# Kernel tuning notes

Hardware: AMD Instinct MI355X
Metric: run time of the kernel (lower is better)

Reference implementation:

```python
import jax, jax.numpy as jnp
import numpy as np

ATT_DIM = 1024
N_HEADS = 16
D_HEAD = ATT_DIM // N_HEADS
LARGE = 1e30  # fp32 masking constant used by masked_softmax


def setup_inputs() -> dict:
    key = jax.random.key(0)
    ks = jax.random.split(key, 12)
    B, Tq, Tv, D = 4, 2048, 2048, 1024
    s = 1.0 / np.sqrt(D)
    sf = 1.0 / np.sqrt(ATT_DIM)
    return {
        "query": jax.random.normal(ks[0], (B, Tq, D), jnp.float32),
        "value": jax.random.normal(ks[1], (B, Tv, D), jnp.float32),
        "value_lens": jax.random.randint(ks[2], (B,), 0, Tv, jnp.int32),
        "Wq": jax.random.normal(ks[3], (D, ATT_DIM), jnp.float32) * s,
        "bq": jnp.zeros((ATT_DIM,), jnp.float32),
        "Wk": jax.random.normal(ks[4], (D, ATT_DIM), jnp.float32) * s,
        "bk": jnp.zeros((ATT_DIM,), jnp.float32),
        "Wv": jax.random.normal(ks[5], (D, ATT_DIM), jnp.float32) * s,
        "bv": jnp.zeros((ATT_DIM,), jnp.float32),
        "Wf": jax.random.normal(ks[6], (ATT_DIM, ATT_DIM), jnp.float32) * sf,
        "bf": jnp.zeros((ATT_DIM,), jnp.float32),
    }


def _attention(query, value, value_lens, Wq, bq, Wk, bk, Wv, bv, Wf, bf):
    B, Tq, _ = query.shape
    Tv = value.shape[1]
    # projections
    k = value @ Wk + bk                     # [B,Tv,att_dim]
    v = value @ Wv + bv                     # [B,Tv,att_dim]
    q = (query @ Wq + bq) / jnp.sqrt(jnp.asarray(D_HEAD, query.dtype))
    # split heads
    q = q.reshape(B, Tq, N_HEADS, D_HEAD)
    k = k.reshape(B, Tv, N_HEADS, D_HEAD)
    v = v.reshape(B, Tv, N_HEADS, D_HEAD)
    # energy: [B, n_heads, Tq, Tv]
    energy = jnp.einsum("bind,bjnd->bnij", q, k)
    # sequence mask: [B,1,1,Tv]
    mask = (jnp.arange(Tv)[None, :] < value_lens[:, None]).astype(energy.dtype)
    energy = energy - (1.0 - mask)[:, None, None, :] * jnp.asarray(LARGE, energy.dtype)
    att_weight = jax.nn.softmax(energy, axis=-1)
    # context: [B, Tq, n_heads, d_head] -> [B, Tq, att_dim]
    context = jnp.einsum("bnij,bjnd->bind", att_weight, v).reshape(B, Tq, ATT_DIM)
    return context @ Wf + bf  # final_att (num_att_head > 1)


def reference(query, value, value_lens, Wq, bq, Wk, bk, Wv, bv, Wf, bf):
    return _attention(query, value, value_lens, Wq, bq, Wk, bk, Wv, bv, Wf, bf)
```

## Files before the change

### kernel.cpp

```cpp
#include <hip/hip_runtime.h>
#include <hip/hip_bf16.h>

typedef __attribute__((ext_vector_type(8))) short short8;
typedef __attribute__((ext_vector_type(4))) short short4b;
typedef __attribute__((ext_vector_type(4))) float f32x4;
typedef unsigned short u16;
typedef unsigned int u32;
typedef __attribute__((ext_vector_type(2))) unsigned int u32x2;
typedef __attribute__((ext_vector_type(8))) unsigned short u16x8;
typedef __attribute__((ext_vector_type(4))) unsigned short u16x4;

__device__ __forceinline__ u16 f2bf(float f) {
    u32 u = __builtin_bit_cast(u32, f);
    u += 0x7FFFu + ((u >> 16) & 1u);
    return (u16)(u >> 16);
}
__device__ __forceinline__ u32 cvtpk(float a, float b) {
    u32 r;
    asm("v_cvt_pk_bf16_f32 %0, %1, %2" : "=v"(r) : "v"(a), "v"(b));
    return r;
}
__device__ __forceinline__ float fexp2(float x) {
    float r;
    asm("v_exp_f32 %0, %1" : "=v"(r) : "v"(x));
    return r;
}
#if defined(__has_builtin)
#if __has_builtin(__builtin_amdgcn_mfma_f32_16x16x16_bf16)
#define MFMA16(a, b, c) __builtin_amdgcn_mfma_f32_16x16x16_bf16((a), (b), (c), 0, 0, 0)
#elif __has_builtin(__builtin_amdgcn_mfma_f32_16x16x16bf16_1k)
#define MFMA16(a, b, c) __builtin_amdgcn_mfma_f32_16x16x16bf16_1k((a), (b), (c), 0, 0, 0)
#endif
#endif
#ifndef MFMA16
__device__ __forceinline__ f32x4 mfma16_asm(short4b a, short4b b, f32x4 c) {
    asm volatile("s_nop 1\n\tv_mfma_f32_16x16x16_bf16 %0, %1, %2, %0"
                 : "+v"(c) : "v"(a), "v"(b));
    return c;
}
#define MFMA16(a, b, c) mfma16_asm((a), (b), (c))
#endif

__device__ __forceinline__ int swz(int row, int col) {
    return (row * 128 + col * 2) ^ ((row & 7) << 4);
}

__device__ __forceinline__ void gl16(const void* g, void* l) {
    __builtin_amdgcn_global_load_lds(
        (const __attribute__((address_space(1))) unsigned int*)g,
        (__attribute__((address_space(3))) unsigned int*)l, 16, 0, 0);
}

#define FENCE() asm volatile("" ::: "memory")
#define BARRIER() do { FENCE(); __builtin_amdgcn_s_barrier(); FENCE(); } while (0)

__global__ __launch_bounds__(256)
void prep_kernel(const float* __restrict__ query, const float* __restrict__ value,
                 u16* __restrict__ qB, u16* __restrict__ vB,
                 const float* __restrict__ W0, const float* __restrict__ W1,
                 const float* __restrict__ W2, const float* __restrict__ W3,
                 u16* __restrict__ T0, u16* __restrict__ T1,
                 u16* __restrict__ T2, u16* __restrict__ T3)
{
    int bid = blockIdx.x;
    if (bid < 8192) {
        const float* src; u16* dst;
        if (bid < 4096) { src = query; dst = qB; }
        else            { src = value; dst = vB; bid -= 4096; }
        const int i = bid * 256 + threadIdx.x;
        const float4 a = ((const float4*)src)[2 * i];
        const float4 b = ((const float4*)src)[2 * i + 1];
        u16x8 h;
        h[0] = f2bf(a.x); h[1] = f2bf(a.y); h[2] = f2bf(a.z); h[3] = f2bf(a.w);
        h[4] = f2bf(b.x); h[5] = f2bf(b.y); h[6] = f2bf(b.z); h[7] = f2bf(b.w);
        ((u16x8*)dst)[i] = h;
        return;
    }
    int b2 = bid - 8192;
    const int z = b2 >> 10; b2 &= 1023;
    const float* W; u16* T;
    switch (z) {
        case 0:  W = W0; T = T0; break;
        case 1:  W = W1; T = T1; break;
        case 2:  W = W2; T = T2; break;
        default: W = W3; T = T3; break;
    }
    __shared__ u16 tile[32][33];
    const int tid = threadIdx.x;
    const int n0 = (b2 & 31) * 32, k0 = (b2 >> 5) * 32;
    const int r = tid >> 3, c = (tid & 7) * 4;
    float4 v = *(const float4*)(W + (size_t)(k0 + r) * 1024 + n0 + c);
    tile[c + 0][r] = f2bf(v.x);
    tile[c + 1][r] = f2bf(v.y);
    tile[c + 2][r] = f2bf(v.z);
    tile[c + 3][r] = f2bf(v.w);
    __syncthreads();
    u16x4 h;
    h[0] = tile[r][c]; h[1] = tile[r][c + 1]; h[2] = tile[r][c + 2]; h[3] = tile[r][c + 3];
    *(u16x4*)(T + (size_t)(n0 + r) * 1024 + k0 + c) = h;
}

#define GNK 32

__device__ __forceinline__ void stage_a(const u16* __restrict__ A, unsigned char* bufA,
                                        int row0, int kt, int tid) {
    const int r = tid >> 2, s = tid & 3;
    gl16((const unsigned char*)A + (size_t)(row0 + r) * 2048 + kt * 64 + ((s ^ (r & 3)) << 4),
         bufA + tid * 16);
}
__device__ __forceinline__ void stage_b(const u16* __restrict__ BT, unsigned char* bufB,
                                        int col0, int kt, int hb, int tid) {
    const int r = hb * 128 + (tid >> 2), s = tid & 3;
    gl16((const unsigned char*)BT + (size_t)(col0 + r) * 2048 + kt * 64 + ((s ^ (r & 3)) << 4),
         bufB + hb * 8192 + tid * 16);
}

__device__ __forceinline__ void gemm_core(const u16* __restrict__ A, const u16* __restrict__ BT,
                                          int row0, int col0, unsigned char* smem,
                                          int tid, int wm, int wn, int l15, int lhi,
                                          f32x4 acc[4][4])
{
    const int slot = (lhi ^ (l15 & 3)) << 4;
    #pragma unroll
    for (int kt = 0; kt < 2; ++kt) {
        unsigned char* buf = smem + kt * 24576;
        stage_a(A, buf, row0, kt, tid);
        stage_b(BT, buf + 8192, col0, kt, 0, tid);
        stage_b(BT, buf + 8192, col0, kt, 1, tid);
    }
    asm volatile("s_waitcnt vmcnt(3)" ::: "memory");
    BARRIER();

    int cb = 0;
    for (int k = 0; k < GNK; ++k) {
        unsigned char* bufA = smem + cb * 24576;
        unsigned char* bufB = bufA + 8192;
        const bool st = (k + 2 < GNK);
        int nb = cb + 2; if (nb >= 3) nb -= 3;
        unsigned char* nbuf = smem + nb * 24576;
        cb = (cb == 2) ? 0 : cb + 1;

        short8 a0, a1, a2, a3, b0, b1;
        a0 = *(const short8*)(bufA + (wm * 64 + 0 * 16 + l15) * 64 + slot);
        a1 = *(const short8*)(bufA + (wm * 64 + 1 * 16 + l15) * 64 + slot);
        a2 = *(const short8*)(bufA + (wm * 64 + 2 * 16 + l15) * 64 + slot);
        a3 = *(const short8*)(bufA + (wm * 64 + 3 * 16 + l15) * 64 + slot);
        b0 = *(const short8*)(bufB + (wn * 64 + 0 * 16 + l15) * 64 + slot);
        b1 = *(const short8*)(bufB + (wn * 64 + 1 * 16 + l15) * 64 + slot);
        if (st) stage_a(A, nbuf, row0, k + 2, tid);
        BARRIER();
        __builtin_amdgcn_s_setprio(1);
        acc[0][0] = __builtin_amdgcn_mfma_f32_16x16x32_bf16(a0, b0, acc[0][0], 0, 0, 0);
        acc[0][1] = __builtin_amdgcn_mfma_f32_16x16x32_bf16(a0, b1, acc[0][1], 0, 0, 0);
        acc[1][0] = __builtin_amdgcn_mfma_f32_16x16x32_bf16(a1, b0, acc[1][0], 0, 0, 0);
        acc[1][1] = __builtin_amdgcn_mfma_f32_16x16x32_bf16(a1, b1, acc[1][1], 0, 0, 0);
        acc[2][0] = __builtin_amdgcn_mfma_f32_16x16x32_bf16(a2, b0, acc[2][0], 0, 0, 0);
        acc[2][1] = __builtin_amdgcn_mfma_f32_16x16x32_bf16(a2, b1, acc[2][1], 0, 0, 0);
        acc[3][0] = __builtin_amdgcn_mfma_f32_16x16x32_bf16(a3, b0, acc[3][0], 0, 0, 0);
        acc[3][1] = __builtin_amdgcn_mfma_f32_16x16x32_bf16(a3, b1, acc[3][1], 0, 0, 0);
        __builtin_amdgcn_s_setprio(0);
        BARRIER();

        short8 b2, b3;
        b2 = *(const short8*)(bufB + (wn * 64 + 2 * 16 + l15) * 64 + slot);
        b3 = *(const short8*)(bufB + (wn * 64 + 3 * 16 + l15) * 64 + slot);
        if (st) {
            stage_b(BT, nbuf + 8192, col0, k + 2, 0, tid);
            stage_b(BT, nbuf + 8192, col0, k + 2, 1, tid);
        }
        if (k < GNK - 2)       asm volatile("s_waitcnt vmcnt(3)" ::: "memory");
        else if (k == GNK - 2) asm volatile("s_waitcnt vmcnt(0)" ::: "memory");
        BARRIER();
        __builtin_amdgcn_s_setprio(1);
        acc[0][2] = __builtin_amdgcn_mfma_f32_16x16x32_bf16(a0, b2, acc[0][2], 0, 0, 0);
        acc[0][3] = __builtin_amdgcn_mfma_f32_16x16x32_bf16(a0, b3, acc[0][3], 0, 0, 0);
        acc[1][2] = __builtin_amdgcn_mfma_f32_16x16x32_bf16(a1, b2, acc[1][2], 0, 0, 0);
        acc[1][3] = __builtin_amdgcn_mfma_f32_16x16x32_bf16(a1, b3, acc[1][3], 0, 0, 0);
        acc[2][2] = __builtin_amdgcn_mfma_f32_16x16x32_bf16(a2, b2, acc[2][2], 0, 0, 0);
        acc[2][3] = __builtin_amdgcn_mfma_f32_16x16x32_bf16(a2, b3, acc[2][3], 0, 0, 0);
        acc[3][2] = __builtin_amdgcn_mfma_f32_16x16x32_bf16(a3, b2, acc[3][2], 0, 0, 0);
        acc[3][3] = __builtin_amdgcn_mfma_f32_16x16x32_bf16(a3, b3, acc[3][3], 0, 0, 0);
        __builtin_amdgcn_s_setprio(0);
        BARRIER();
    }
}

__global__ __launch_bounds__(512, 4)
void proj_kernel(const u16* __restrict__ queryB, const u16* __restrict__ valueB,
                 const u16* __restrict__ WqT, const u16* __restrict__ WkT,
                 const u16* __restrict__ WvT,
                 const float* __restrict__ bq, const float* __restrict__ bk,
                 const float* __restrict__ bv,
                 u16* __restrict__ Qb, u16* __restrict__ Kb, u16* __restrict__ Vt)
{
    __shared__ __align__(16) unsigned char smem[73728];
    const int t = (blockIdx.x & 7) * 96 + (blockIdx.x >> 3);
    const int z = t >> 8;
    const int tile = t & 255;
    const int row0 = (tile >> 2) * 128, col0 = (tile & 3) * 256;

    const u16* A    = (z == 0) ? queryB : valueB;
    const u16* BT   = (z == 0) ? WqT : (z == 1) ? WkT : WvT;
    const float* bias = (z == 0) ? bq : (z == 1) ? bk : bv;

    const int tid = threadIdx.x;
    const int lane = tid & 63, w = tid >> 6;
    const int wm = w >> 2, wn = w & 3;
    const int l15 = lane & 15, lhi = lane >> 4;

    f32x4 acc[4][4];
    const f32x4 fz = {0.f, 0.f, 0.f, 0.f};
    #pragma unroll
    for (int m = 0; m < 4; ++m)
        #pragma unroll
        for (int n = 0; n < 4; ++n) acc[m][n] = fz;

    gemm_core(A, BT, row0, col0, smem, tid, wm, wn, l15, lhi, acc);

    if (z < 2) {
        u16* out = (z == 0) ? Qb : Kb;
        const float scale = (z == 0) ? 0.18033688011112042f : 1.0f;
        const int bb = row0 >> 11;
        #pragma unroll
        for (int n = 0; n < 4; ++n) {
            int col = col0 + wn * 64 + n * 16 + l15;
            int hh = col >> 6, d = col & 63;
            float bv2 = bias[col];
            #pragma unroll
            for (int m = 0; m < 4; ++m) {
                int rbase = row0 + wm * 64 + m * 16 + lhi * 4;
                #pragma unroll
                for (int rr = 0; rr < 4; ++rr) {
                    int trow = (rbase + rr) & 2047;
                    out[(((size_t)bb * 16 + hh) * 2048 + trow) * 64 + d] =
                        f2bf((acc[m][n][rr] + bv2) * scale);
                }
            }
        }
    } else {
        __syncthreads();
        u16* vl = (u16*)smem;
        #pragma unroll
        for (int n = 0; n < 4; ++n) {
            int c = wn * 64 + n * 16 + l15;
            float bv2 = bias[col0 + c];
            #pragma unroll
            for (int m = 0; m < 4; ++m) {
                int rl = wm * 64 + m * 16 + lhi * 4;
                u16x4 h;
                #pragma unroll
                for (int rr = 0; rr < 4; ++rr) h[rr] = f2bf(acc[m][n][rr] + bv2);
                *(u16x4*)(vl + c * 132 + rl) = h;
            }
        }
        __syncthreads();
        const int bb = row0 >> 11, t0 = row0 & 2047;
        const int c = tid >> 1, hseg = tid & 1;
        const int col = col0 + c;
        const int hh = col >> 6, d = col & 63;
        size_t gb = (((size_t)bb * 16 + hh) * 64 + d) * 2048 + t0 + hseg * 64;
        #pragma unroll
        for (int j = 0; j < 8; ++j) {
            u16x8 v = *(const u16x8*)(vl + c * 132 + hseg * 64 + j * 8);
            *(u16x8*)(Vt + gb + j * 8) = v;
        }
    }
}

__global__ __launch_bounds__(512, 4)
void fgemm_kernel(const u16* __restrict__ Ctx, const u16* __restrict__ WfT,
                  const float* __restrict__ bias, float* __restrict__ out)
{
    __shared__ __align__(16) unsigned char smem[73728];
    const int t = (blockIdx.x & 7) * 32 + (blockIdx.x >> 3);
    const int row0 = (t >> 2) * 128, col0 = (t & 3) * 256;

    const int tid = threadIdx.x;
    const int lane = tid & 63, w = tid >> 6;
    const int wm = w >> 2, wn = w & 3;
    const int l15 = lane & 15, lhi = lane >> 4;

    f32x4 acc[4][4];
    const f32x4 fz = {0.f, 0.f, 0.f, 0.f};
    #pragma unroll
    for (int m = 0; m < 4; ++m)
        #pragma unroll
        for (int n = 0; n < 4; ++n) acc[m][n] = fz;

    gemm_core(Ctx, WfT, row0, col0, smem, tid, wm, wn, l15, lhi, acc);

    #pragma unroll
    for (int n = 0; n < 4; ++n) {
        int col = col0 + wn * 64 + n * 16 + l15;
        float bv2 = bias[col];
        #pragma unroll
        for (int m = 0; m < 4; ++m) {
            int rbase = row0 + wm * 64 + m * 16 + lhi * 4;
            #pragma unroll
            for (int rr = 0; rr < 4; ++rr)
                out[(size_t)(rbase + rr) * 1024 + col] = acc[m][n][rr] + bv2;
        }
    }
}

__global__ __launch_bounds__(512, 4)
void attn_kernel(const u16* __restrict__ Qb, const u16* __restrict__ Kb,
                 const u16* __restrict__ Vt, const int* __restrict__ lens,
                 u16* __restrict__ Ctx)
{
    __shared__ __align__(16) unsigned char ksm[2][8192];
    __shared__ __align__(16) unsigned char vsm[2][8192];

    const int tid = threadIdx.x;
    const int lane = tid & 63;
    const int w = tid >> 6;
    const int l15 = lane & 15, lhi = lane >> 4;
    const int u = blockIdx.x;
    const int b = (u >> 8) & 3;
    const int v = u & 255;
    const int qt = (v >> 3) & 15;
    const int hh = ((v >> 7) & 1) * 8 + (v & 7);
    const size_t head = (size_t)(b * 16 + hh);
    const unsigned char* Kbase = (const unsigned char*)Kb + head * (2048 * 128);
    const unsigned char* Vbase = (const unsigned char*)Vt + head * (2048 * 128);
    const unsigned char* Qbase = (const unsigned char*)Qb + head * (2048 * 128) + (size_t)qt * (128 * 128);

    const int o0 = w * 1024 + lane * 16;
    const int r0 = o0 >> 7;
    const int sc0 = (o0 & 127) ^ ((r0 & 7) << 4);

    const unsigned char* kp = Kbase + (size_t)r0 * 128 + sc0;
    const unsigned char* vp = Vbase + (size_t)r0 * 4096 + sc0;

    const int lens_b = lens[b];
    const bool uniform = (lens_b == 0);
    const int len = uniform ? 2048 : lens_b;
    const int nt = (len + 63) >> 6;
    const bool tail = (!uniform) && ((len & 63) != 0);

    auto stage = [&](int t, int bi) {
        gl16(kp + (size_t)t * 8192, ksm[bi] + o0);
        gl16(vp + (size_t)t * 128, vsm[bi] + o0);
    };
    stage(0, 0);

    short8 qa[2];
    #pragma unroll
    for (int ks = 0; ks < 2; ++ks)
        qa[ks] = *(const short8*)(Qbase + (w * 16 + l15) * 128 + ks * 64 + lhi * 16);

    short4b ones16;
    #pragma unroll
    for (int i = 0; i < 4; ++i) ones16[i] = (short)0x3F80;

    __syncthreads();

    float m = -1e30f;
    const f32x4 fz = {0.f, 0.f, 0.f, 0.f};
    f32x4 cs = fz;
    f32x4 cT[4];
    #pragma unroll
    for (int nf = 0; nf < 4; ++nf) cT[nf] = fz;

    for (int t = 0; t < nt; ++t) {
        const int cur = t & 1;
        if (t + 1 < nt) stage(t + 1, cur ^ 1);

        f32x4 s[4];
        #pragma unroll
        for (int jf = 0; jf < 4; ++jf) s[jf] = fz;
        if (!uniform) {
            __builtin_amdgcn_s_setprio(1);
            #pragma unroll
            for (int ks = 0; ks < 2; ++ks)
                #pragma unroll
                for (int jf = 0; jf < 4; ++jf) {
                    short8 kb = *(const short8*)(ksm[cur] + swz(jf * 16 + l15, ks * 32 + lhi * 8));
                    s[jf] = __builtin_amdgcn_mfma_f32_16x16x32_bf16(kb, qa[ks], s[jf], 0, 0, 0);
                }
            __builtin_amdgcn_s_setprio(0);
            if (tail && t == nt - 1) {
                const int kvb = t * 64 + lhi * 4;
                #pragma unroll
                for (int jf = 0; jf < 4; ++jf)
                    #pragma unroll
                    for (int r = 0; r < 4; ++r)
                        if (kvb + jf * 16 + r >= len) s[jf][r] = -1e30f;
            }
        }
        f32x4 m4;
        #pragma unroll
        for (int r = 0; r < 4; ++r)
            m4[r] = fmaxf(fmaxf(s[0][r], s[1][r]), fmaxf(s[2][r], s[3][r]));
        float tmax = fmaxf(fmaxf(m4[0], m4[1]), fmaxf(m4[2], m4[3]));
        tmax = fmaxf(tmax, __shfl_xor(tmax, 16));
        tmax = fmaxf(tmax, __shfl_xor(tmax, 32));
        if (__any(tmax > m + 8.f)) {
            const float mnew = fmaxf(m, tmax);
            const float sc = fexp2(m - mnew);
            #pragma unroll
            for (int r = 0; r < 4; ++r) cs[r] *= sc;
            #pragma unroll
            for (int nf = 0; nf < 4; ++nf)
                #pragma unroll
                for (int r = 0; r < 4; ++r) cT[nf][r] *= sc;
            m = mnew;
        }
        #pragma unroll
        for (int jf = 0; jf < 4; ++jf)
            #pragma unroll
            for (int r = 0; r < 4; ++r)
                s[jf][r] = fexp2(s[jf][r] - m);
        short4b pf[4];
        #pragma unroll
        for (int jf = 0; jf < 4; ++jf) {
            u32x2 t2 = { cvtpk(s[jf][0], s[jf][1]), cvtpk(s[jf][2], s[jf][3]) };
            pf[jf] = __builtin_bit_cast(short4b, t2);
        }
        __builtin_amdgcn_s_setprio(1);
        #pragma unroll
        for (int jf = 0; jf < 4; ++jf) {
            cs = MFMA16(ones16, pf[jf], cs);
            #pragma unroll
            for (int nf = 0; nf < 4; ++nf) {
                short4b vb = *(const short4b*)(vsm[cur] + swz(nf * 16 + l15, jf * 16 + lhi * 4));
                cT[nf] = MFMA16(vb, pf[jf], cT[nf]);
            }
        }
        __builtin_amdgcn_s_setprio(0);
        __syncthreads();
    }

    asm volatile("s_nop 7");
    const float inv = 1.0f / cs[0];
    const int trow = qt * 128 + w * 16 + l15;
    u16* op = Ctx + ((size_t)b * 2048 + trow) * 1024 + hh * 64 + lhi * 4;
    #pragma unroll
    for (int nf = 0; nf < 4; ++nf) {
        u16x4 h;
        #pragma unroll
        for (int r = 0; r < 4; ++r) h[r] = f2bf(cT[nf][r] * inv);
        *(u16x4*)(op + nf * 16) = h;
    }
}

extern "C" void kernel_launch(void* const* d_in, const int* in_sizes, int n_in,
                              void* d_out, int out_size, void* d_ws, size_t ws_size,
                              hipStream_t stream)
{
    (void)in_sizes; (void)n_in; (void)out_size; (void)ws_size;
    const float* query = (const float*)d_in[0];
    const float* value = (const float*)d_in[1];
    const int*   lens  = (const int*)d_in[2];
    const float* Wq = (const float*)d_in[3];
    const float* bq = (const float*)d_in[4];
    const float* Wk = (const float*)d_in[5];
    const float* bk = (const float*)d_in[6];
    const float* Wv = (const float*)d_in[7];
    const float* bv = (const float*)d_in[8];
    const float* Wf = (const float*)d_in[9];
    const float* bfp = (const float*)d_in[10];

    unsigned char* ws = (unsigned char*)d_ws;
    const size_t MB = (size_t)1 << 20;
    u16* WqT = (u16*)(ws + 0 * MB);
    u16* WkT = (u16*)(ws + 2 * MB);
    u16* WvT = (u16*)(ws + 4 * MB);
    u16* WfT = (u16*)(ws + 6 * MB);
    u16* Qb  = (u16*)(ws + 8 * MB);
    u16* Kb  = (u16*)(ws + 24 * MB);
    u16* Vt  = (u16*)(ws + 40 * MB);
    u16* Ctx = (u16*)(ws + 56 * MB);

    u16* queryB = (u16*)d_out;
    u16* valueB = queryB + (size_t)8192 * 1024;

    prep_kernel<<<dim3(12288), dim3(256), 0, stream>>>(query, value, queryB, valueB,
                                                       Wq, Wk, Wv, Wf, WqT, WkT, WvT, WfT);

    proj_kernel<<<dim3(768), dim3(512), 0, stream>>>(queryB, valueB, WqT, WkT, WvT,
                                                     bq, bk, bv, Qb, Kb, Vt);

    attn_kernel<<<dim3(1024), dim3(512), 0, stream>>>(Qb, Kb, Vt, lens, Ctx);

    fgemm_kernel<<<dim3(256), dim3(512), 0, stream>>>(Ctx, WfT, bfp, (float*)d_out);
}
```

Baseline: 173.9 us.

## Shrink GEMM tiles to 128x128 and simplify the pipeline to one barrier phase

The projection and final GEMMs now use 128x128 output tiles instead of 128x256, which doubles the grid size (1536 and 512 blocks) and cuts shared memory per block from 72KB to 48KB. The K-loop is restructured so that all loads for a stage are issued up front, followed by a single wait and barrier per iteration, instead of two split phases. The aim is better occupancy and load balance across CUs, especially for the 256-block final GEMM. The cost is lower data reuse per tile, which means more global and L2 traffic for the B operand.

After: 180.8 us. +4.0%, slower.

```diff
diff --git a/kernel.cpp b/kernel.cpp
--- a/kernel.cpp
+++ b/kernel.cpp
@@ -102,53 +102,53 @@
 
 #define GNK 32
 
-__device__ __forceinline__ void stage_a(const u16* __restrict__ A, unsigned char* bufA,
-                                        int row0, int kt, int tid) {
+__device__ __forceinline__ void stg_a(const u16* __restrict__ A, unsigned char* buf,
+                                      int row0, int kt, int tid) {
     const int r = tid >> 2, s = tid & 3;
     gl16((const unsigned char*)A + (size_t)(row0 + r) * 2048 + kt * 64 + ((s ^ (r & 3)) << 4),
-         bufA + tid * 16);
-}
-__device__ __forceinline__ void stage_b(const u16* __restrict__ BT, unsigned char* bufB,
-                                        int col0, int kt, int hb, int tid) {
-    const int r = hb * 128 + (tid >> 2), s = tid & 3;
+         buf + tid * 16);
+}
+__device__ __forceinline__ void stg_b(const u16* __restrict__ BT, unsigned char* buf,
+                                      int col0, int kt, int tid) {
+    const int r = tid >> 2, s = tid & 3;
     gl16((const unsigned char*)BT + (size_t)(col0 + r) * 2048 + kt * 64 + ((s ^ (r & 3)) << 4),
-         bufB + hb * 8192 + tid * 16);
-}
-
-__device__ __forceinline__ void gemm_core(const u16* __restrict__ A, const u16* __restrict__ BT,
-                                          int row0, int col0, unsigned char* smem,
-                                          int tid, int wm, int wn, int l15, int lhi,
-                                          f32x4 acc[4][4])
+         buf + 8192 + tid * 16);
+}
+
+__device__ __forceinline__ void gemm128(const u16* __restrict__ A, const u16* __restrict__ BT,
+                                        int row0, int col0, unsigned char* smem,
+                                        int tid, int wm, int wn, int l15, int lhi,
+                                        f32x4 acc[4][2])
 {
     const int slot = (lhi ^ (l15 & 3)) << 4;
-    #pragma unroll
-    for (int kt = 0; kt < 2; ++kt) {
-        unsigned char* buf = smem + kt * 24576;
-        stage_a(A, buf, row0, kt, tid);
-        stage_b(BT, buf + 8192, col0, kt, 0, tid);
-        stage_b(BT, buf + 8192, col0, kt, 1, tid);
-    }
-    asm volatile("s_waitcnt vmcnt(3)" ::: "memory");
+    stg_a(A, smem, row0, 0, tid);
+    stg_b(BT, smem, col0, 0, tid);
+    stg_a(A, smem + 16384, row0, 1, tid);
+    stg_b(BT, smem + 16384, col0, 1, tid);
+    asm volatile("s_waitcnt vmcnt(2)" ::: "memory");
     BARRIER();
 
     int cb = 0;
     for (int k = 0; k < GNK; ++k) {
-        unsigned char* bufA = smem + cb * 24576;
+        unsigned char* bufA = smem + cb * 16384;
         unsigned char* bufB = bufA + 8192;
-        const bool st = (k + 2 < GNK);
         int nb = cb + 2; if (nb >= 3) nb -= 3;
-        unsigned char* nbuf = smem + nb * 24576;
         cb = (cb == 2) ? 0 : cb + 1;
-
+        if (k + 2 < GNK) {
+            unsigned char* nbuf = smem + nb * 16384;
+            stg_a(A, nbuf, row0, k + 2, tid);
+            stg_b(BT, nbuf, col0, k + 2, tid);
+        }
+        if (k < GNK - 2)       asm volatile("s_waitcnt vmcnt(2)" ::: "memory");
+        else if (k == GNK - 2) asm volatile("s_waitcnt vmcnt(0)" ::: "memory");
+        BARRIER();
         short8 a0, a1, a2, a3, b0, b1;
         a0 = *(const short8*)(bufA + (wm * 64 + 0 * 16 + l15) * 64 + slot);
         a1 = *(const short8*)(bufA + (wm * 64 + 1 * 16 + l15) * 64 + slot);
         a2 = *(const short8*)(bufA + (wm * 64 + 2 * 16 + l15) * 64 + slot);
         a3 = *(const short8*)(bufA + (wm * 64 + 3 * 16 + l15) * 64 + slot);
-        b0 = *(const short8*)(bufB + (wn * 64 + 0 * 16 + l15) * 64 + slot);
-        b1 = *(const short8*)(bufB + (wn * 64 + 1 * 16 + l15) * 64 + slot);
-        if (st) stage_a(A, nbuf, row0, k + 2, tid);
-        BARRIER();
+        b0 = *(const short8*)(bufB + (wn * 32 + 0 * 16 + l15) * 64 + slot);
+        b1 = *(const short8*)(bufB + (wn * 32 + 1 * 16 + l15) * 64 + slot);
         __builtin_amdgcn_s_setprio(1);
         acc[0][0] = __builtin_amdgcn_mfma_f32_16x16x32_bf16(a0, b0, acc[0][0], 0, 0, 0);
         acc[0][1] = __builtin_amdgcn_mfma_f32_16x16x32_bf16(a0, b1, acc[0][1], 0, 0, 0);
@@ -160,28 +160,6 @@
         acc[3][1] = __builtin_amdgcn_mfma_f32_16x16x32_bf16(a3, b1, acc[3][1], 0, 0, 0);
         __builtin_amdgcn_s_setprio(0);
         BARRIER();
-
-        short8 b2, b3;
-        b2 = *(const short8*)(bufB + (wn * 64 + 2 * 16 + l15) * 64 + slot);
-        b3 = *(const short8*)(bufB + (wn * 64 + 3 * 16 + l15) * 64 + slot);
-        if (st) {
-            stage_b(BT, nbuf + 8192, col0, k + 2, 0, tid);
-            stage_b(BT, nbuf + 8192, col0, k + 2, 1, tid);
-        }
-        if (k < GNK - 2)       asm volatile("s_waitcnt vmcnt(3)" ::: "memory");
-        else if (k == GNK - 2) asm volatile("s_waitcnt vmcnt(0)" ::: "memory");
-        BARRIER();
-        __builtin_amdgcn_s_setprio(1);
-        acc[0][2] = __builtin_amdgcn_mfma_f32_16x16x32_bf16(a0, b2, acc[0][2], 0, 0, 0);
-        acc[0][3] = __builtin_amdgcn_mfma_f32_16x16x32_bf16(a0, b3, acc[0][3], 0, 0, 0);
-        acc[1][2] = __builtin_amdgcn_mfma_f32_16x16x32_bf16(a1, b2, acc[1][2], 0, 0, 0);
-        acc[1][3] = __builtin_amdgcn_mfma_f32_16x16x32_bf16(a1, b3, acc[1][3], 0, 0, 0);
-        acc[2][2] = __builtin_amdgcn_mfma_f32_16x16x32_bf16(a2, b2, acc[2][2], 0, 0, 0);
-        acc[2][3] = __builtin_amdgcn_mfma_f32_16x16x32_bf16(a2, b3, acc[2][3], 0, 0, 0);
-        acc[3][2] = __builtin_amdgcn_mfma_f32_16x16x32_bf16(a3, b2, acc[3][2], 0, 0, 0);
-        acc[3][3] = __builtin_amdgcn_mfma_f32_16x16x32_bf16(a3, b3, acc[3][3], 0, 0, 0);
-        __builtin_amdgcn_s_setprio(0);
-        BARRIER();
     }
 }
 
@@ -193,11 +171,11 @@
                  const float* __restrict__ bv,
                  u16* __restrict__ Qb, u16* __restrict__ Kb, u16* __restrict__ Vt)
 {
-    __shared__ __align__(16) unsigned char smem[73728];
-    const int t = (blockIdx.x & 7) * 96 + (blockIdx.x >> 3);
-    const int z = t >> 8;
-    const int tile = t & 255;
-    const int row0 = (tile >> 2) * 128, col0 = (tile & 3) * 256;
+    __shared__ __align__(16) unsigned char smem[49152];
+    const int t = (blockIdx.x & 7) * 192 + (blockIdx.x >> 3);
+    const int z = t >> 9;
+    const int tile = t & 511;
+    const int row0 = (tile >> 3) * 128, col0 = (tile & 7) * 128;
 
     const u16* A    = (z == 0) ? queryB : valueB;
     const u16* BT   = (z == 0) ? WqT : (z == 1) ? WkT : WvT;
@@ -208,22 +186,22 @@
     const int wm = w >> 2, wn = w & 3;
     const int l15 = lane & 15, lhi = lane >> 4;
 
-    f32x4 acc[4][4];
+    f32x4 acc[4][2];
     const f32x4 fz = {0.f, 0.f, 0.f, 0.f};
     #pragma unroll
     for (int m = 0; m < 4; ++m)
         #pragma unroll
-        for (int n = 0; n < 4; ++n) acc[m][n] = fz;
-
-    gemm_core(A, BT, row0, col0, smem, tid, wm, wn, l15, lhi, acc);
+        for (int n = 0; n < 2; ++n) acc[m][n] = fz;
+
+    gemm128(A, BT, row0, col0, smem, tid, wm, wn, l15, lhi, acc);
 
     if (z < 2) {
         u16* out = (z == 0) ? Qb : Kb;
         const float scale = (z == 0) ? 0.18033688011112042f : 1.0f;
         const int bb = row0 >> 11;
         #pragma unroll
-        for (int n = 0; n < 4; ++n) {
-            int col = col0 + wn * 64 + n * 16 + l15;
+        for (int n = 0; n < 2; ++n) {
+            int col = col0 + wn * 32 + n * 16 + l15;
             int hh = col >> 6, d = col & 63;
             float bv2 = bias[col];
             #pragma unroll
@@ -241,26 +219,26 @@
         __syncthreads();
         u16* vl = (u16*)smem;
         #pragma unroll
-        for (int n = 0; n < 4; ++n) {
-            int c = wn * 64 + n * 16 + l15;
+        for (int n = 0; n < 2; ++n) {
+            int c = wn * 32 + n * 16 + l15;
             float bv2 = bias[col0 + c];
             #pragma unroll
             for (int m = 0; m < 4; ++m) {
                 int rl = wm * 64 + m * 16 + lhi * 4;
-                u16x4 h;
+                u16x4 hv;
                 #pragma unroll
-                for (int rr = 0; rr < 4; ++rr) h[rr] = f2bf(acc[m][n][rr] + bv2);
-                *(u16x4*)(vl + c * 132 + rl) = h;
+                for (int rr = 0; rr < 4; ++rr) hv[rr] = f2bf(acc[m][n][rr] + bv2);
+                *(u16x4*)(vl + c * 132 + rl) = hv;
             }
         }
         __syncthreads();
         const int bb = row0 >> 11, t0 = row0 & 2047;
-        const int c = tid >> 1, hseg = tid & 1;
+        const int c = tid >> 2, hseg = tid & 1, jh = (tid >> 1) & 1;
         const int col = col0 + c;
         const int hh = col >> 6, d = col & 63;
         size_t gb = (((size_t)bb * 16 + hh) * 64 + d) * 2048 + t0 + hseg * 64;
         #pragma unroll
-        for (int j = 0; j < 8; ++j) {
+        for (int j = jh * 4; j < jh * 4 + 4; ++j) {
             u16x8 v = *(const u16x8*)(vl + c * 132 + hseg * 64 + j * 8);
             *(u16x8*)(Vt + gb + j * 8) = v;
         }
@@ -271,27 +249,27 @@
 void fgemm_kernel(const u16* __restrict__ Ctx, const u16* __restrict__ WfT,
                   const float* __restrict__ bias, float* __restrict__ out)
 {
-    __shared__ __align__(16) unsigned char smem[73728];
-    const int t = (blockIdx.x & 7) * 32 + (blockIdx.x >> 3);
-    const int row0 = (t >> 2) * 128, col0 = (t & 3) * 256;
+    __shared__ __align__(16) unsigned char smem[49152];
+    const int t = (blockIdx.x & 7) * 64 + (blockIdx.x >> 3);
+    const int row0 = (t >> 3) * 128, col0 = (t & 7) * 128;
 
     const int tid = threadIdx.x;
     const int lane = tid & 63, w = tid >> 6;
     const int wm = w >> 2, wn = w & 3;
     const int l15 = lane & 15, lhi = lane >> 4;
 
-    f32x4 acc[4][4];
+    f32x4 acc[4][2];
     const f32x4 fz = {0.f, 0.f, 0.f, 0.f};
     #pragma unroll
     for (int m = 0; m < 4; ++m)
         #pragma unroll
-        for (int n = 0; n < 4; ++n) acc[m][n] = fz;
-
-    gemm_core(Ctx, WfT, row0, col0, smem, tid, wm, wn, l15, lhi, acc);
-
-    #pragma unroll
-    for (int n = 0; n < 4; ++n) {
-        int col = col0 + wn * 64 + n * 16 + l15;
+        for (int n = 0; n < 2; ++n) acc[m][n] = fz;
+
+    gemm128(Ctx, WfT, row0, col0, smem, tid, wm, wn, l15, lhi, acc);
+
+    #pragma unroll
+    for (int n = 0; n < 2; ++n) {
+        int col = col0 + wn * 32 + n * 16 + l15;
         float bv2 = bias[col];
         #pragma unroll
         for (int m = 0; m < 4; ++m) {
@@ -478,10 +456,10 @@
     prep_kernel<<<dim3(12288), dim3(256), 0, stream>>>(query, value, queryB, valueB,
                                                        Wq, Wk, Wv, Wf, WqT, WkT, WvT, WfT);
 
-    proj_kernel<<<dim3(768), dim3(512), 0, stream>>>(queryB, valueB, WqT, WkT, WvT,
-                                                     bq, bk, bv, Qb, Kb, Vt);
+    proj_kernel<<<dim3(1536), dim3(512), 0, stream>>>(queryB, valueB, WqT, WkT, WvT,
+                                                      bq, bk, bv, Qb, Kb, Vt);
 
     attn_kernel<<<dim3(1024), dim3(512), 0, stream>>>(Qb, Kb, Vt, lens, Ctx);
 
-    fgemm_kernel<<<dim3(256), dim3(512), 0, stream>>>(Ctx, WfT, bfp, (float*)d_out);
-}
+    fgemm_kernel<<<dim3(512), dim3(512), 0, stream>>>(Ctx, WfT, bfp, (float*)d_out);
+}
```

## Schedule attention tiles through an atomic work queue, longest batches first

Applied to the files above, without the earlier changes.

The attention kernel no longer maps each block to a fixed (batch, head, q-tile). Blocks now pull tile indices from a global atomic counter, and tiles are ordered so that batches with the most KV tiles (from value_lens) are handed out first. The aim is to reduce load imbalance and tail idle time, since KV lengths differ per batch. The cost is an atomic plus an extra barrier per tile, a changed head/q-tile traversal order that may affect L2 reuse, and a completion counter that resets state on the assumption that exactly 1024 blocks run.

Result: slower. 194.2 us (+11.6%).

```diff
diff --git a/kernel.cpp b/kernel.cpp
--- a/kernel.cpp
+++ b/kernel.cpp
@@ -53,6 +53,9 @@
 
 #define FENCE() asm volatile("" ::: "memory")
 #define BARRIER() do { FENCE(); __builtin_amdgcn_s_barrier(); FENCE(); } while (0)
+
+__device__ u32 g_qctr = 0;
+__device__ u32 g_done = 0;
 
 __global__ __launch_bounds__(256)
 void prep_kernel(const float* __restrict__ query, const float* __restrict__ value,
@@ -310,137 +313,166 @@
 {
     __shared__ __align__(16) unsigned char ksm[2][8192];
     __shared__ __align__(16) unsigned char vsm[2][8192];
+    __shared__ int sj;
 
     const int tid = threadIdx.x;
     const int lane = tid & 63;
     const int w = tid >> 6;
     const int l15 = lane & 15, lhi = lane >> 4;
-    const int u = blockIdx.x;
-    const int b = (u >> 8) & 3;
-    const int v = u & 255;
-    const int qt = (v >> 3) & 15;
-    const int hh = ((v >> 7) & 1) * 8 + (v & 7);
-    const size_t head = (size_t)(b * 16 + hh);
-    const unsigned char* Kbase = (const unsigned char*)Kb + head * (2048 * 128);
-    const unsigned char* Vbase = (const unsigned char*)Vt + head * (2048 * 128);
-    const unsigned char* Qbase = (const unsigned char*)Qb + head * (2048 * 128) + (size_t)qt * (128 * 128);
 
     const int o0 = w * 1024 + lane * 16;
     const int r0 = o0 >> 7;
     const int sc0 = (o0 & 127) ^ ((r0 & 7) << 4);
 
-    const unsigned char* kp = Kbase + (size_t)r0 * 128 + sc0;
-    const unsigned char* vp = Vbase + (size_t)r0 * 4096 + sc0;
-
-    const int lens_b = lens[b];
-    const bool uniform = (lens_b == 0);
-    const int len = uniform ? 2048 : lens_b;
-    const int nt = (len + 63) >> 6;
-    const bool tail = (!uniform) && ((len & 63) != 0);
-
-    auto stage = [&](int t, int bi) {
-        gl16(kp + (size_t)t * 8192, ksm[bi] + o0);
-        gl16(vp + (size_t)t * 128, vsm[bi] + o0);
-    };
-    stage(0, 0);
-
-    short8 qa[2];
-    #pragma unroll
-    for (int ks = 0; ks < 2; ++ks)
-        qa[ks] = *(const short8*)(Qbase + (w * 16 + l15) * 128 + ks * 64 + lhi * 16);
+    int ntv[4];
+    #pragma unroll
+    for (int b = 0; b < 4; ++b) {
+        int lb = lens[b];
+        int ln = (lb == 0) ? 2048 : lb;
+        ntv[b] = (ln + 63) >> 6;
+    }
+    int ordv[4] = {0, 1, 2, 3};
+    #pragma unroll
+    for (int i = 0; i < 3; ++i)
+        #pragma unroll
+        for (int k2 = 0; k2 < 3 - i; ++k2)
+            if (ntv[ordv[k2]] < ntv[ordv[k2 + 1]]) {
+                int tmp = ordv[k2]; ordv[k2] = ordv[k2 + 1]; ordv[k2 + 1] = tmp;
+            }
 
     short4b ones16;
     #pragma unroll
     for (int i = 0; i < 4; ++i) ones16[i] = (short)0x3F80;
-
-    __syncthreads();
-
-    float m = -1e30f;
     const f32x4 fz = {0.f, 0.f, 0.f, 0.f};
-    f32x4 cs = fz;
-    f32x4 cT[4];
-    #pragma unroll
-    for (int nf = 0; nf < 4; ++nf) cT[nf] = fz;
-
-    for (int t = 0; t < nt; ++t) {
-        const int cur = t & 1;
-        if (t + 1 < nt) stage(t + 1, cur ^ 1);
-
-        f32x4 s[4];
-        #pragma unroll
-        for (int jf = 0; jf < 4; ++jf) s[jf] = fz;
-        if (!uniform) {
+
+    for (;;) {
+        if (tid == 0) sj = (int)atomicAdd(&g_qctr, 1u);
+        __syncthreads();
+        const int j = sj;
+        if (j >= 1024) break;
+
+        const int b = ordv[j >> 8];
+        const int v = j & 255;
+        const int hh = v >> 4;
+        const int qt = v & 15;
+        const size_t head = (size_t)(b * 16 + hh);
+        const unsigned char* Qbase = (const unsigned char*)Qb + head * (2048 * 128) + (size_t)qt * (128 * 128);
+        const unsigned char* kp = (const unsigned char*)Kb + head * (2048 * 128) + (size_t)r0 * 128 + sc0;
+        const unsigned char* vp = (const unsigned char*)Vt + head * (2048 * 128) + (size_t)r0 * 4096 + sc0;
+
+        const int lens_b = lens[b];
+        const bool uniform = (lens_b == 0);
+        const int len = uniform ? 2048 : lens_b;
+        const int nt = (len + 63) >> 6;
+        const bool tail = (!uniform) && ((len & 63) != 0);
+
+        auto stage = [&](int t, int bi) {
+            gl16(kp + (size_t)t * 8192, ksm[bi] + o0);
+            gl16(vp + (size_t)t * 128, vsm[bi] + o0);
+        };
+        stage(0, 0);
+
+        short8 qa[2];
+        #pragma unroll
+        for (int ks = 0; ks < 2; ++ks)
+            qa[ks] = *(const short8*)(Qbase + (w * 16 + l15) * 128 + ks * 64 + lhi * 16);
+
+        float m = -1e30f;
+        f32x4 cs = fz;
+        f32x4 cT[4];
+        #pragma unroll
+        for (int nf = 0; nf < 4; ++nf) cT[nf] = fz;
+
+        __syncthreads();
+
+        for (int t = 0; t < nt; ++t) {
+            const int cur = t & 1;
+            if (t + 1 < nt) stage(t + 1, cur ^ 1);
+
+            f32x4 s[4];
+            #pragma unroll
+            for (int jf = 0; jf < 4; ++jf) s[jf] = fz;
+            if (!uniform) {
+                __builtin_amdgcn_s_setprio(1);
+                #pragma unroll
+                for (int ks = 0; ks < 2; ++ks)
+                    #pragma unroll
+                    for (int jf = 0; jf < 4; ++jf) {
+                        short8 kb = *(const short8*)(ksm[cur] + swz(jf * 16 + l15, ks * 32 + lhi * 8));
+                        s[jf] = __builtin_amdgcn_mfma_f32_16x16x32_bf16(kb, qa[ks], s[jf], 0, 0, 0);
+                    }
+                __builtin_amdgcn_s_setprio(0);
+                if (tail && t == nt - 1) {
+                    const int kvb = t * 64 + lhi * 4;
+                    #pragma unroll
+                    for (int jf = 0; jf < 4; ++jf)
+                        #pragma unroll
+                        for (int r = 0; r < 4; ++r)
+                            if (kvb + jf * 16 + r >= len) s[jf][r] = -1e30f;
+                }
+            }
+            f32x4 m4;
+            #pragma unroll
+            for (int r = 0; r < 4; ++r)
+                m4[r] = fmaxf(fmaxf(s[0][r], s[1][r]), fmaxf(s[2][r], s[3][r]));
+            float tmax = fmaxf(fmaxf(m4[0], m4[1]), fmaxf(m4[2], m4[3]));
+            tmax = fmaxf(tmax, __shfl_xor(tmax, 16));
+            tmax = fmaxf(tmax, __shfl_xor(tmax, 32));
+            if (__any(tmax > m + 8.f)) {
+                const float mnew = fmaxf(m, tmax);
+                const float sc = fexp2(m - mnew);
+                #pragma unroll
+                for (int r = 0; r < 4; ++r) cs[r] *= sc;
+                #pragma unroll
+                for (int nf = 0; nf < 4; ++nf)
+                    #pragma unroll
+                    for (int r = 0; r < 4; ++r) cT[nf][r] *= sc;
+                m = mnew;
+            }
+            #pragma unroll
+            for (int jf = 0; jf < 4; ++jf)
+                #pragma unroll
+                for (int r = 0; r < 4; ++r)
+                    s[jf][r] = fexp2(s[jf][r] - m);
+            short4b pf[4];
+            #pragma unroll
+            for (int jf = 0; jf < 4; ++jf) {
+                u32x2 t2 = { cvtpk(s[jf][0], s[jf][1]), cvtpk(s[jf][2], s[jf][3]) };
+                pf[jf] = __builtin_bit_cast(short4b, t2);
+            }
             __builtin_amdgcn_s_setprio(1);
             #pragma unroll
-            for (int ks = 0; ks < 2; ++ks)
-                #pragma unroll
-                for (int jf = 0; jf < 4; ++jf) {
-                    short8 kb = *(const short8*)(ksm[cur] + swz(jf * 16 + l15, ks * 32 + lhi * 8));
-                    s[jf] = __builtin_amdgcn_mfma_f32_16x16x32_bf16(kb, qa[ks], s[jf], 0, 0, 0);
+            for (int jf = 0; jf < 4; ++jf) {
+                cs = MFMA16(ones16, pf[jf], cs);
+                #pragma unroll
+                for (int nf = 0; nf < 4; ++nf) {
+                    short4b vb = *(const short4b*)(vsm[cur] + swz(nf * 16 + l15, jf * 16 + lhi * 4));
+                    cT[nf] = MFMA16(vb, pf[jf], cT[nf]);
                 }
+            }
             __builtin_amdgcn_s_setprio(0);
-            if (tail && t == nt - 1) {
-                const int kvb = t * 64 + lhi * 4;
-                #pragma unroll
-                for (int jf = 0; jf < 4; ++jf)
-                    #pragma unroll
-                    for (int r = 0; r < 4; ++r)
-                        if (kvb + jf * 16 + r >= len) s[jf][r] = -1e30f;
-            }
-        }
-        f32x4 m4;
-        #pragma unroll
-        for (int r = 0; r < 4; ++r)
-            m4[r] = fmaxf(fmaxf(s[0][r], s[1][r]), fmaxf(s[2][r], s[3][r]));
-        float tmax = fmaxf(fmaxf(m4[0], m4[1]), fmaxf(m4[2], m4[3]));
-        tmax = fmaxf(tmax, __shfl_xor(tmax, 16));
-        tmax = fmaxf(tmax, __shfl_xor(tmax, 32));
-        if (__any(tmax > m + 8.f)) {
-            const float mnew = fmaxf(m, tmax);
-            const float sc = fexp2(m - mnew);
-            #pragma unroll
-            for (int r = 0; r < 4; ++r) cs[r] *= sc;
-            #pragma unroll
-            for (int nf = 0; nf < 4; ++nf)
-                #pragma unroll
-                for (int r = 0; r < 4; ++r) cT[nf][r] *= sc;
-            m = mnew;
-        }
-        #pragma unroll
-        for (int jf = 0; jf < 4; ++jf)
-            #pragma unroll
-            for (int r = 0; r < 4; ++r)
-                s[jf][r] = fexp2(s[jf][r] - m);
-        short4b pf[4];
-        #pragma unroll
-        for (int jf = 0; jf < 4; ++jf) {
-            u32x2 t2 = { cvtpk(s[jf][0], s[jf][1]), cvtpk(s[jf][2], s[jf][3]) };
-            pf[jf] = __builtin_bit_cast(short4b, t2);
-        }
-        __builtin_amdgcn_s_setprio(1);
-        #pragma unroll
-        for (int jf = 0; jf < 4; ++jf) {
-            cs = MFMA16(ones16, pf[jf], cs);
-            #pragma unroll
-            for (int nf = 0; nf < 4; ++nf) {
-                short4b vb = *(const short4b*)(vsm[cur] + swz(nf * 16 + l15, jf * 16 + lhi * 4));
-                cT[nf] = MFMA16(vb, pf[jf], cT[nf]);
-            }
-        }
-        __builtin_amdgcn_s_setprio(0);
-        __syncthreads();
-    }
-
-    asm volatile("s_nop 7");
-    const float inv = 1.0f / cs[0];
-    const int trow = qt * 128 + w * 16 + l15;
-    u16* op = Ctx + ((size_t)b * 2048 + trow) * 1024 + hh * 64 + lhi * 4;
-    #pragma unroll
-    for (int nf = 0; nf < 4; ++nf) {
-        u16x4 h;
-        #pragma unroll
-        for (int r = 0; r < 4; ++r) h[r] = f2bf(cT[nf][r] * inv);
-        *(u16x4*)(op + nf * 16) = h;
+            __syncthreads();
+        }
+
+        asm volatile("s_nop 7");
+        const float inv = 1.0f / cs[0];
+        const int trow = qt * 128 + w * 16 + l15;
+        u16* op = Ctx + ((size_t)b * 2048 + trow) * 1024 + hh * 64 + lhi * 4;
+        #pragma unroll
+        for (int nf = 0; nf < 4; ++nf) {
+            u16x4 h;
+            #pragma unroll
+            for (int r = 0; r < 4; ++r) h[r] = f2bf(cT[nf][r] * inv);
+            *(u16x4*)(op + nf * 16) = h;
+        }
+    }
+
+    if (tid == 0) {
+        u32 old = atomicAdd(&g_done, 1u);
+        if (old == 1023u) {
+            atomicExch(&g_qctr, 0u);
+            atomicExch(&g_done, 0u);
+        }
     }
 }
 
```
